# Performance work log

Measured on AMD Instinct MI355X. Metric: run time of the kernel, lower is better.

## Reference

```python
import jax, jax.numpy as jnp
import numpy as np

B, S, D, H = 4, 2048, 1024, 16
HD = D // H
MASK_VAL = -1e6  # d2l masked_softmax fill value


def setup_inputs() -> dict:
    key = jax.random.key(0)
    ks = jax.random.split(key, 8)
    scale = 1.0 / np.sqrt(D)
    return {
        "queries": jax.random.normal(ks[0], (B, S, D), dtype=jnp.float32),
        "keys": jax.random.normal(ks[1], (B, S, D), dtype=jnp.float32),
        "values": jax.random.normal(ks[2], (B, S, D), dtype=jnp.float32),
        "valid_lens": jax.random.randint(ks[3], (B,), 1, S + 1, dtype=jnp.int32),
        "Wq": jax.random.normal(ks[4], (D, D), dtype=jnp.float32) * scale,
        "Wk": jax.random.normal(ks[5], (D, D), dtype=jnp.float32) * scale,
        "Wv": jax.random.normal(ks[6], (D, D), dtype=jnp.float32) * scale,
        "Wo": jax.random.normal(ks[7], (D, D), dtype=jnp.float32) * scale,
    }


def reference(queries, keys, values, valid_lens, Wq, Wk, Wv, Wo):
    # QKV projections (no bias), then split into heads: [B,S,D] -> [B,H,S,HD]
    def split_heads(x):
        return x.reshape(B, S, H, HD).transpose(0, 2, 1, 3)

    q = split_heads(queries @ Wq)
    k = split_heads(keys @ Wk)
    v = split_heads(values @ Wv)

    # scaled dot-product scores: [B,H,Sq,Sk]
    scores = jnp.einsum('bhqd,bhkd->bhqk', q, k) / jnp.sqrt(jnp.float32(HD))

    # masked softmax over key axis: positions >= valid_len get -1e6 (d2l semantics)
    kv_pos = jnp.arange(S)  # [S]
    mask = kv_pos[None, :] < valid_lens[:, None]  # [B,S]
    scores = jnp.where(mask[:, None, None, :], scores, MASK_VAL)
    attn = jax.nn.softmax(scores, axis=-1)  # dropout=0.0 -> identity

    # weighted sum and merge heads: [B,H,S,HD] -> [B,S,D]
    out = jnp.einsum('bhqk,bhkd->bhqd', attn, v)
    out = out.transpose(0, 2, 1, 3).reshape(B, S, D)
    return out @ Wo
```

## Files before the change

### kernel.cpp

```cpp
#include <hip/hip_runtime.h>
#include <hip/hip_bf16.h>
#include <cstdint>
#include <cstddef>


typedef __hip_bfloat16 bf16;
typedef unsigned short u16;
typedef __attribute__((ext_vector_type(8))) unsigned short ushort8_t;
typedef __attribute__((ext_vector_type(8))) __bf16 bf16x8;
typedef __attribute__((ext_vector_type(4))) float f32x4;

constexpr int Bn = 4, Sn = 2048, Dn = 1024, Hn = 16, HDn = 64;
constexpr size_t BSD = (size_t)Bn * Sn * Dn;
constexpr size_t DD  = (size_t)Dn * Dn;

__device__ __forceinline__ u16 f2b(float f) {
    union { bf16 h; u16 u; } c; c.h = __float2bfloat16(f); return c.u;
}

__device__ __forceinline__ bf16x8 cvt_bf8(f32x4 lo, f32x4 hi) {
    union { ushort8_t u; bf16x8 b; } c;
    c.u[0] = f2b(lo[0]); c.u[1] = f2b(lo[1]); c.u[2] = f2b(lo[2]); c.u[3] = f2b(lo[3]);
    c.u[4] = f2b(hi[0]); c.u[5] = f2b(hi[1]); c.u[6] = f2b(hi[2]); c.u[7] = f2b(hi[3]);
    return c.b;
}

__device__ __forceinline__ void gl_lds16(const void* g, void* l) {
    __builtin_amdgcn_global_load_lds(
        (const __attribute__((address_space(1))) uint32_t*)g,
        (__attribute__((address_space(3))) uint32_t*)l, 16, 0, 0);
}

__global__ __launch_bounds__(256) void transpose_w(
    const float* __restrict__ S0, const float* __restrict__ S1, const float* __restrict__ S2,
    u16* __restrict__ D0, u16* __restrict__ D1, u16* __restrict__ D2)
{
    __shared__ u16 tl[32][33];
    const int z = blockIdx.z;
    const float* S = (z == 0) ? S0 : ((z == 1) ? S1 : S2);
    u16*         D = (z == 0) ? D0 : ((z == 1) ? D1 : D2);
    const int k0 = blockIdx.y * 32, n0 = blockIdx.x * 32;
    const int t = threadIdx.x;
    const int r = t >> 3, c0 = (t & 7) * 4;
    float4 v = *(const float4*)(S + (size_t)(k0 + r) * Dn + n0 + c0);
    tl[r][c0] = f2b(v.x); tl[r][c0 + 1] = f2b(v.y);
    tl[r][c0 + 2] = f2b(v.z); tl[r][c0 + 3] = f2b(v.w);
    __syncthreads();
    ushort4 o;
    o.x = tl[c0][r]; o.y = tl[c0 + 1][r]; o.z = tl[c0 + 2][r]; o.w = tl[c0 + 3][r];
    *(ushort4*)(D + (size_t)(n0 + r) * Dn + k0 + c0) = o;
}

__global__ __launch_bounds__(256) void gemm_qkv(
    const float* __restrict__ A0, const float* __restrict__ A1, const float* __restrict__ A2,
    const u16* __restrict__ B0, const u16* __restrict__ B1, const u16* __restrict__ B2,
    u16* __restrict__ C0, u16* __restrict__ C1, u16* __restrict__ C2, float qscale)
{
    constexpr int K = Dn, BK = 32, BM = 128;
    const int z = blockIdx.z;
    const float* A  = (z == 0) ? A0 : ((z == 1) ? A1 : A2);
    const u16*   Bt = (z == 0) ? B0 : ((z == 1) ? B1 : B2);
    u16*         C  = (z == 0) ? C0 : ((z == 1) ? C1 : C2);
    const float scale = (z == 0) ? qscale : 1.0f;

    __shared__ __attribute__((aligned(16))) float As32[BM][BK];
    __shared__ __attribute__((aligned(16))) u16   Bs[BM][BK];

    const int t = threadIdx.x, l = t & 63, w = t >> 6;
    const int i = l & 15, j = l >> 4;

    const int wl   = blockIdx.x * 64 + blockIdx.y;
    const int col0 = (wl & 7) * BM;
    const int row0 = (wl >> 3) * BM;
    const int m_off = (w & 1) * 64, n_off = (w >> 1) * 64;

    const size_t a_base = (size_t)(row0 + w * 32 + (l >> 3)) * K
                          + (size_t)(((l & 7) ^ (l >> 3)) * 4);
    const size_t b_base = (size_t)(col0 + w * 32 + (l >> 2)) * K
                          + (size_t)((l & 3) * 8);
    float* a_lds = &As32[w * 32][0];
    u16*   b_lds = &Bs[w * 32][0];

    f32x4 acc[4][4] = {};

    for (int k0 = 0; k0 < K; k0 += BK) {
        __syncthreads();
        #pragma unroll
        for (int c = 0; c < 4; c++)
            gl_lds16(A + a_base + (size_t)c * 8 * K + k0, a_lds + c * 8 * BK);
        #pragma unroll
        for (int c = 0; c < 2; c++)
            gl_lds16(Bt + b_base + (size_t)c * 16 * K + k0, b_lds + c * 16 * BK);
        __syncthreads();

        bf16x8 af[4], bfr[4];
        const int xa = i & 7;
        #pragma unroll
        for (int mi = 0; mi < 4; mi++) {
            const float* rp = &As32[m_off + mi * 16 + i][0];
            f32x4 lo = *(const f32x4*)(rp + ((2 * j)     ^ xa) * 4);
            f32x4 hi = *(const f32x4*)(rp + ((2 * j + 1) ^ xa) * 4);
            af[mi] = cvt_bf8(lo, hi);
        }
        #pragma unroll
        for (int ni = 0; ni < 4; ni++)
            bfr[ni] = *(const bf16x8*)&Bs[n_off + ni * 16 + i][j * 8];
        #pragma unroll
        for (int mi = 0; mi < 4; mi++)
            #pragma unroll
            for (int ni = 0; ni < 4; ni++)
                acc[mi][ni] = __builtin_amdgcn_mfma_f32_16x16x32_bf16(
                    af[mi], bfr[ni], acc[mi][ni], 0, 0, 0);
    }

    #pragma unroll
    for (int mi = 0; mi < 4; mi++) {
        #pragma unroll
        for (int r = 0; r < 4; r++) {
            const int m = row0 + m_off + mi * 16 + j * 4 + r;
            const int b = m >> 11, s = m & (Sn - 1);
            #pragma unroll
            for (int ni = 0; ni < 4; ni++) {
                const int n = col0 + n_off + ni * 16 + i;
                const int h = n >> 6, hd = n & (HDn - 1);
                C[(((size_t)(b * Hn + h)) * Sn + s) * HDn + hd] = f2b(acc[mi][ni][r] * scale);
            }
        }
    }
}

__global__ __launch_bounds__(256) void gemm_out(
    const u16* __restrict__ A, const u16* __restrict__ Bt, float* __restrict__ C)
{
    constexpr int K = Dn, BK = 32, BM = 128;
    __shared__ __attribute__((aligned(16))) u16 As[BM][BK];
    __shared__ __attribute__((aligned(16))) u16 Bs[BM][BK];

    const int t = threadIdx.x, l = t & 63, w = t >> 6;
    const int i = l & 15, j = l >> 4;
    const int wl   = blockIdx.x * 64 + blockIdx.y;
    const int col0 = (wl & 7) * BM;
    const int row0 = (wl >> 3) * BM;
    const int m_off = (w & 1) * 64, n_off = (w >> 1) * 64;

    const size_t a_base = (size_t)(row0 + w * 32 + (l >> 2)) * K + (size_t)((l & 3) * 8);
    const size_t b_base = (size_t)(col0 + w * 32 + (l >> 2)) * K + (size_t)((l & 3) * 8);
    u16* a_lds = &As[w * 32][0];
    u16* b_lds = &Bs[w * 32][0];

    f32x4 acc[4][4] = {};

    for (int k0 = 0; k0 < K; k0 += BK) {
        __syncthreads();
        #pragma unroll
        for (int c = 0; c < 2; c++)
            gl_lds16(A + a_base + (size_t)c * 16 * K + k0, a_lds + c * 16 * BK);
        #pragma unroll
        for (int c = 0; c < 2; c++)
            gl_lds16(Bt + b_base + (size_t)c * 16 * K + k0, b_lds + c * 16 * BK);
        __syncthreads();

        bf16x8 af[4], bfr[4];
        #pragma unroll
        for (int mi = 0; mi < 4; mi++)
            af[mi] = *(const bf16x8*)&As[m_off + mi * 16 + i][j * 8];
        #pragma unroll
        for (int ni = 0; ni < 4; ni++)
            bfr[ni] = *(const bf16x8*)&Bs[n_off + ni * 16 + i][j * 8];
        #pragma unroll
        for (int mi = 0; mi < 4; mi++)
            #pragma unroll
            for (int ni = 0; ni < 4; ni++)
                acc[mi][ni] = __builtin_amdgcn_mfma_f32_16x16x32_bf16(
                    af[mi], bfr[ni], acc[mi][ni], 0, 0, 0);
    }

    #pragma unroll
    for (int mi = 0; mi < 4; mi++) {
        #pragma unroll
        for (int r = 0; r < 4; r++) {
            const int m = row0 + m_off + mi * 16 + j * 4 + r;
            #pragma unroll
            for (int ni = 0; ni < 4; ni++) {
                const int n = col0 + n_off + ni * 16 + i;
                C[(size_t)m * Dn + n] = acc[mi][ni][r];
            }
        }
    }
}

__global__ __launch_bounds__(512) void attn_mfma(
    const u16* __restrict__ Qh, const u16* __restrict__ Kh, const u16* __restrict__ Vh,
    const int* __restrict__ vlen, u16* __restrict__ Out)
{
    constexpr int TQ = 128, TK = 64;
    __shared__ __attribute__((aligned(16))) u16 Ks[TK][HDn + 8];
    __shared__ __attribute__((aligned(16))) u16 Vt[HDn][TK + 8];
    __shared__ __attribute__((aligned(16))) u16 Ps[TQ][TK + 8];

    const int t = threadIdx.x, l = t & 63, w = t >> 6;
    const int i = l & 15, j = l >> 4;

    const int b    = blockIdx.x & 3;
    const int rest = blockIdx.x >> 2;
    const int h    = rest & 15;
    const int qt   = rest >> 4;
    const int q0   = qt * TQ;
    const int vl   = vlen[b];

    const size_t hoff = ((size_t)(b * Hn + h)) * Sn * HDn;
    const u16* Qg = Qh + hoff + (size_t)q0 * HDn;
    const u16* Kg = Kh + hoff;
    const u16* Vg = Vh + hoff;

    bf16x8 qf[2];
    #pragma unroll
    for (int ks = 0; ks < 2; ks++)
        qf[ks] = *(const bf16x8*)(Qg + (size_t)(w * 16 + i) * HDn + ks * 32 + j * 8);

    f32x4 acc_o[4] = {};
    float l_part[4] = {0.f, 0.f, 0.f, 0.f};

    const int ntiles = (vl + TK - 1) / TK;

    for (int kt = 0; kt < ntiles; kt++) {
        const int ks0 = kt * TK;
        __syncthreads();
        {
            const int kr = t >> 3, kc = (t & 7) * 8;
            *(ushort8_t*)&Ks[kr][kc] =
                *(const ushort8_t*)(Kg + (size_t)(ks0 + kr) * HDn + kc);
        }
        {
            const int vr = (t >> 4) * 2, dc = (t & 15) * 4;
            ushort4 v0 = *(const ushort4*)(Vg + (size_t)(ks0 + vr) * HDn + dc);
            ushort4 v1 = *(const ushort4*)(Vg + (size_t)(ks0 + vr + 1) * HDn + dc);
            *(ushort2*)&Vt[dc + 0][vr] = make_ushort2(v0.x, v1.x);
            *(ushort2*)&Vt[dc + 1][vr] = make_ushort2(v0.y, v1.y);
            *(ushort2*)&Vt[dc + 2][vr] = make_ushort2(v0.z, v1.z);
            *(ushort2*)&Vt[dc + 3][vr] = make_ushort2(v0.w, v1.w);
        }
        __syncthreads();

        f32x4 s[4] = {};
        #pragma unroll
        for (int ks = 0; ks < 2; ks++) {
            bf16x8 kf[4];
            #pragma unroll
            for (int ni = 0; ni < 4; ni++)
                kf[ni] = *(const bf16x8*)&Ks[ni * 16 + i][ks * 32 + j * 8];
            #pragma unroll
            for (int ni = 0; ni < 4; ni++)
                s[ni] = __builtin_amdgcn_mfma_f32_16x16x32_bf16(
                    qf[ks], kf[ni], s[ni], 0, 0, 0);
        }

        const bool tail = (ks0 + TK > vl);
        #pragma unroll
        for (int ni = 0; ni < 4; ni++) {
            const bool keep = !tail || (ks0 + ni * 16 + i < vl);
            #pragma unroll
            for (int r = 0; r < 4; r++) {
                float p = __expf(s[ni][r]);
                p = keep ? p : 0.0f;
                l_part[r] += p;
                Ps[w * 16 + j * 4 + r][ni * 16 + i] = f2b(p);
            }
        }

        #pragma unroll
        for (int ks = 0; ks < 2; ks++) {
            bf16x8 pa = *(const bf16x8*)&Ps[w * 16 + i][ks * 32 + j * 8];
            bf16x8 vb[4];
            #pragma unroll
            for (int di = 0; di < 4; di++)
                vb[di] = *(const bf16x8*)&Vt[di * 16 + i][ks * 32 + j * 8];
            #pragma unroll
            for (int di = 0; di < 4; di++)
                acc_o[di] = __builtin_amdgcn_mfma_f32_16x16x32_bf16(
                    pa, vb[di], acc_o[di], 0, 0, 0);
        }
    }

    #pragma unroll
    for (int r = 0; r < 4; r++) {
        float v = l_part[r];
        #pragma unroll
        for (int d = 1; d < 16; d <<= 1) v += __shfl_xor(v, d, 64);
        l_part[r] = v;
    }

    #pragma unroll
    for (int r = 0; r < 4; r++) {
        const int q = q0 + w * 16 + j * 4 + r;
        const float inv = 1.0f / l_part[r];
        #pragma unroll
        for (int di = 0; di < 4; di++) {
            const int d = di * 16 + i;
            Out[((size_t)b * Sn + q) * Dn + h * HDn + d] = f2b(acc_o[di][r] * inv);
        }
    }
}

extern "C" void kernel_launch(void* const* d_in, const int* in_sizes, int n_in,
                              void* d_out, int out_size, void* d_ws, size_t ws_size,
                              hipStream_t stream)
{
    const float* xq = (const float*)d_in[0];
    const float* xk = (const float*)d_in[1];
    const float* xv = (const float*)d_in[2];
    const int*   vl = (const int*)d_in[3];
    const float* Wq = (const float*)d_in[4];
    const float* Wk = (const float*)d_in[5];
    const float* Wv = (const float*)d_in[6];
    const float* Wo = (const float*)d_in[7];
    float* out = (float*)d_out;

    u16* Qh = (u16*)d_ws;
    u16* Kh = Qh + BSD;
    u16* Vh = Kh + BSD;
    u16* Ao = Vh + BSD;
    u16* WtQ = Ao;
    u16* WtK = WtQ + DD;
    u16* WtV = WtK + DD;
    u16* WoT = Qh;

    transpose_w<<<dim3(32, 32, 3), 256, 0, stream>>>(Wq, Wk, Wv, WtQ, WtK, WtV);
    gemm_qkv<<<dim3(8, 64, 3), 256, 0, stream>>>(xq, xk, xv, WtQ, WtK, WtV,
                                                 Qh, Kh, Vh, 0.125f);
    attn_mfma<<<dim3(Bn * Hn * (Sn / 128)), 512, 0, stream>>>(Qh, Kh, Vh, vl, Ao);
    transpose_w<<<dim3(32, 32, 1), 256, 0, stream>>>(Wo, Wo, Wo, WoT, WoT, WoT);
    gemm_out<<<dim3(8, 64), 256, 0, stream>>>(Ao, WoT, out);
}
```

Baseline: 386.9 us.

## Double-buffer LDS tiles in QKV and output projection GEMMs

Both projection GEMMs now use two LDS buffers and issue the global-to-LDS loads for the next K tile before computing on the current one. The loop needs one barrier per iteration instead of two, and load latency can overlap with MFMA work. In exchange the LDS footprint doubles, which may reduce occupancy. The async loads may also not be waited on correctly if the barrier does not wait for the direct-to-LDS transfers.

```diff
diff --git a/kernel.cpp b/kernel.cpp
--- a/kernel.cpp
+++ b/kernel.cpp
@@ -56,15 +56,15 @@
     const u16* __restrict__ B0, const u16* __restrict__ B1, const u16* __restrict__ B2,
     u16* __restrict__ C0, u16* __restrict__ C1, u16* __restrict__ C2, float qscale)
 {
-    constexpr int K = Dn, BK = 32, BM = 128;
+    constexpr int K = Dn, BK = 32, BM = 128, NT = K / BK;
     const int z = blockIdx.z;
     const float* A  = (z == 0) ? A0 : ((z == 1) ? A1 : A2);
     const u16*   Bt = (z == 0) ? B0 : ((z == 1) ? B1 : B2);
     u16*         C  = (z == 0) ? C0 : ((z == 1) ? C1 : C2);
     const float scale = (z == 0) ? qscale : 1.0f;
 
-    __shared__ __attribute__((aligned(16))) float As32[BM][BK];
-    __shared__ __attribute__((aligned(16))) u16   Bs[BM][BK];
+    __shared__ __attribute__((aligned(16))) float As32[2][BM][BK];
+    __shared__ __attribute__((aligned(16))) u16   Bs[2][BM][BK];
 
     const int t = threadIdx.x, l = t & 63, w = t >> 6;
     const int i = l & 15, j = l >> 4;
@@ -78,39 +78,47 @@
                           + (size_t)(((l & 7) ^ (l >> 3)) * 4);
     const size_t b_base = (size_t)(col0 + w * 32 + (l >> 2)) * K
                           + (size_t)((l & 3) * 8);
-    float* a_lds = &As32[w * 32][0];
-    u16*   b_lds = &Bs[w * 32][0];
+
+    auto stage = [&](int buf, int kk) {
+        float* al = &As32[buf][w * 32][0];
+        u16*   bl = &Bs[buf][w * 32][0];
+        #pragma unroll
+        for (int c = 0; c < 4; c++)
+            gl_lds16(A + a_base + (size_t)c * 8 * K + kk, al + c * 8 * BK);
+        #pragma unroll
+        for (int c = 0; c < 2; c++)
+            gl_lds16(Bt + b_base + (size_t)c * 16 * K + kk, bl + c * 16 * BK);
+    };
 
     f32x4 acc[4][4] = {};
 
-    for (int k0 = 0; k0 < K; k0 += BK) {
-        __syncthreads();
-        #pragma unroll
-        for (int c = 0; c < 4; c++)
-            gl_lds16(A + a_base + (size_t)c * 8 * K + k0, a_lds + c * 8 * BK);
-        #pragma unroll
-        for (int c = 0; c < 2; c++)
-            gl_lds16(Bt + b_base + (size_t)c * 16 * K + k0, b_lds + c * 16 * BK);
-        __syncthreads();
+    stage(0, 0);
+    __syncthreads();
+
+    for (int kt = 0; kt < NT; kt++) {
+        const int cur = kt & 1, nxt = cur ^ 1;
+        if (kt + 1 < NT) stage(nxt, (kt + 1) * BK);
 
         bf16x8 af[4], bfr[4];
         const int xa = i & 7;
         #pragma unroll
         for (int mi = 0; mi < 4; mi++) {
-            const float* rp = &As32[m_off + mi * 16 + i][0];
+            const float* rp = &As32[cur][m_off + mi * 16 + i][0];
             f32x4 lo = *(const f32x4*)(rp + ((2 * j)     ^ xa) * 4);
             f32x4 hi = *(const f32x4*)(rp + ((2 * j + 1) ^ xa) * 4);
             af[mi] = cvt_bf8(lo, hi);
         }
         #pragma unroll
         for (int ni = 0; ni < 4; ni++)
-            bfr[ni] = *(const bf16x8*)&Bs[n_off + ni * 16 + i][j * 8];
+            bfr[ni] = *(const bf16x8*)&Bs[cur][n_off + ni * 16 + i][j * 8];
         #pragma unroll
         for (int mi = 0; mi < 4; mi++)
             #pragma unroll
             for (int ni = 0; ni < 4; ni++)
                 acc[mi][ni] = __builtin_amdgcn_mfma_f32_16x16x32_bf16(
                     af[mi], bfr[ni], acc[mi][ni], 0, 0, 0);
+
+        __syncthreads();
     }
 
     #pragma unroll
@@ -132,9 +140,9 @@
 __global__ __launch_bounds__(256) void gemm_out(
     const u16* __restrict__ A, const u16* __restrict__ Bt, float* __restrict__ C)
 {
-    constexpr int K = Dn, BK = 32, BM = 128;
-    __shared__ __attribute__((aligned(16))) u16 As[BM][BK];
-    __shared__ __attribute__((aligned(16))) u16 Bs[BM][BK];
+    constexpr int K = Dn, BK = 32, BM = 128, NT = K / BK;
+    __shared__ __attribute__((aligned(16))) u16 As[2][BM][BK];
+    __shared__ __attribute__((aligned(16))) u16 Bs[2][BM][BK];
 
     const int t = threadIdx.x, l = t & 63, w = t >> 6;
     const int i = l & 15, j = l >> 4;
@@ -145,34 +153,42 @@
 
     const size_t a_base = (size_t)(row0 + w * 32 + (l >> 2)) * K + (size_t)((l & 3) * 8);
     const size_t b_base = (size_t)(col0 + w * 32 + (l >> 2)) * K + (size_t)((l & 3) * 8);
-    u16* a_lds = &As[w * 32][0];
-    u16* b_lds = &Bs[w * 32][0];
+
+    auto stage = [&](int buf, int kk) {
+        u16* al = &As[buf][w * 32][0];
+        u16* bl = &Bs[buf][w * 32][0];
+        #pragma unroll
+        for (int c = 0; c < 2; c++)
+            gl_lds16(A + a_base + (size_t)c * 16 * K + kk, al + c * 16 * BK);
+        #pragma unroll
+        for (int c = 0; c < 2; c++)
+            gl_lds16(Bt + b_base + (size_t)c * 16 * K + kk, bl + c * 16 * BK);
+    };
 
     f32x4 acc[4][4] = {};
 
-    for (int k0 = 0; k0 < K; k0 += BK) {
-        __syncthreads();
-        #pragma unroll
-        for (int c = 0; c < 2; c++)
-            gl_lds16(A + a_base + (size_t)c * 16 * K + k0, a_lds + c * 16 * BK);
-        #pragma unroll
-        for (int c = 0; c < 2; c++)
-            gl_lds16(Bt + b_base + (size_t)c * 16 * K + k0, b_lds + c * 16 * BK);
-        __syncthreads();
+    stage(0, 0);
+    __syncthreads();
+
+    for (int kt = 0; kt < NT; kt++) {
+        const int cur = kt & 1, nxt = cur ^ 1;
+        if (kt + 1 < NT) stage(nxt, (kt + 1) * BK);
 
         bf16x8 af[4], bfr[4];
         #pragma unroll
         for (int mi = 0; mi < 4; mi++)
-            af[mi] = *(const bf16x8*)&As[m_off + mi * 16 + i][j * 8];
+            af[mi] = *(const bf16x8*)&As[cur][m_off + mi * 16 + i][j * 8];
         #pragma unroll
         for (int ni = 0; ni < 4; ni++)
-            bfr[ni] = *(const bf16x8*)&Bs[n_off + ni * 16 + i][j * 8];
+            bfr[ni] = *(const bf16x8*)&Bs[cur][n_off + ni * 16 + i][j * 8];
         #pragma unroll
         for (int mi = 0; mi < 4; mi++)
             #pragma unroll
             for (int ni = 0; ni < 4; ni++)
                 acc[mi][ni] = __builtin_amdgcn_mfma_f32_16x16x32_bf16(
                     af[mi], bfr[ni], acc[mi][ni], 0, 0, 0);
+
+        __syncthreads();
     }
 
     #pragma unroll
```

Result: slower. 419.9 us (+8.5%).
